# Performance work log

Hardware: AMD Instinct MI355X
Metric: run time of the kernel (lower is better)

## Reference

```python
import jax, jax.numpy as jnp
import numpy as np

D_MODEL = 1024
N_HEAD = 16
DK = D_MODEL // N_HEAD
D_FF = 2048
EPS = 1e-6
NEG = -1e10


def layer_norm(x, gamma, beta):
    # torch .std() is unbiased (N-1), and eps is added to std (not var)
    mean = jnp.mean(x, axis=-1, keepdims=True)
    var = jnp.sum((x - mean) ** 2, axis=-1, keepdims=True) / (x.shape[-1] - 1)
    std = jnp.sqrt(var)
    return gamma * (x - mean) / (std + EPS) + beta


def setup_inputs() -> dict:
    key = jax.random.key(0)
    ks = jax.random.split(key, 12)
    s = 0.02
    inp = {
        'x': jax.random.normal(ks[0], (16, 512, D_MODEL), dtype=jnp.float32),
        'x_mask': jax.random.randint(ks[1], (16, 1, 1, 512), 0, 2, dtype=jnp.int32),
        'Wq': jax.random.normal(ks[2], (D_MODEL, D_MODEL), dtype=jnp.float32) * s,
        'bq': jnp.zeros((D_MODEL,), jnp.float32),
        'Wk': jax.random.normal(ks[3], (D_MODEL, D_MODEL), dtype=jnp.float32) * s,
        'bk': jnp.zeros((D_MODEL,), jnp.float32),
        'Wv': jax.random.normal(ks[4], (D_MODEL, D_MODEL), dtype=jnp.float32) * s,
        'bv': jnp.zeros((D_MODEL,), jnp.float32),
        'Wo': jax.random.normal(ks[5], (D_MODEL, D_MODEL), dtype=jnp.float32) * s,
        'bo': jnp.zeros((D_MODEL,), jnp.float32),
        'gamma1': jnp.ones((D_MODEL,), jnp.float32),
        'beta1': jnp.zeros((D_MODEL,), jnp.float32),
        'W1': jax.random.normal(ks[6], (D_MODEL, D_FF), dtype=jnp.float32) * s,
        'b1': jnp.zeros((D_FF,), jnp.float32),
        'W2': jax.random.normal(ks[7], (D_FF, D_MODEL), dtype=jnp.float32) * s,
        'b2': jnp.zeros((D_MODEL,), jnp.float32),
        'gamma2': jnp.ones((D_MODEL,), jnp.float32),
        'beta2': jnp.zeros((D_MODEL,), jnp.float32),
    }
    return inp


def reference(x, x_mask, Wq, bq, Wk, bk, Wv, bv, Wo, bo, gamma1, beta1,
              W1, b1, W2, b2, gamma2, beta2):
    B, S, _ = x.shape
    # QKV projections -> [B, S, H, DK]
    q = (x @ Wq + bq).reshape(B, S, N_HEAD, DK)
    k = (x @ Wk + bk).reshape(B, S, N_HEAD, DK)
    v = (x @ Wv + bv).reshape(B, S, N_HEAD, DK)
    # scores [B, H, Sq, Sk]
    scores = jnp.einsum('bqhd,bkhd->bhqk', q, k) / jnp.sqrt(jnp.float32(DK))
    scores = jnp.where(x_mask == 0, jnp.float32(NEG), scores)
    probs = jax.nn.softmax(scores, axis=-1)
    attn = jnp.einsum('bhqk,bkhd->bqhd', probs, v).reshape(B, S, D_MODEL)
    attn_out = attn @ Wo + bo
    # residual + post-LN 1
    h = layer_norm(attn_out + x, gamma1, beta1)
    # FFN (exact GELU as torch nn.GELU default)
    ffn = jax.nn.gelu(h @ W1 + b1, approximate=False) @ W2 + b2
    out = layer_norm(ffn + h, gamma2, beta2)
    return out
```

## Files before the change

kernel.cpp:

```cpp
#include <hip/hip_runtime.h>
#include <math.h>

#define B_ 16
#define S_ 512
#define DM 1024
#define NH 16
#define DFF 2048

typedef short bf16x8 __attribute__((ext_vector_type(8)));
typedef float f32x4 __attribute__((ext_vector_type(4)));
typedef unsigned short u16;

__device__ __forceinline__ u16 f2bf(float f) {
  unsigned int u = __float_as_uint(f);
  u += 0x7FFF + ((u >> 16) & 1);
  return (u16)(u >> 16);
}

__device__ __forceinline__ unsigned cvtpk_bf16(float lo, float hi) {
  unsigned r;
  asm("v_cvt_pk_bf16_f32 %0, %1, %2" : "=v"(r) : "v"(lo), "v"(hi));
  return r;
}

__device__ __forceinline__ float gelu_exact(float x) {
  return 0.5f * x * (1.0f + erff(x * 0.70710678118654752f));
}

__device__ __forceinline__ void gload_lds16(const void* g, void* l) {
  __builtin_amdgcn_global_load_lds((const __attribute__((address_space(1))) void*)g,
                                   (__attribute__((address_space(3))) void*)l, 16, 0, 0);
}

#define QSCALE 0.18033688011112042f
#define MASKNEG -1.442695e10f


__global__ void cvt_bf16_k(const float* __restrict__ in, u16* __restrict__ out, int n) {
  int i = (blockIdx.x * blockDim.x + threadIdx.x) * 4;
  float4 v = *(const float4*)(in + i);
  uint2 pk;
  pk.x = (unsigned)f2bf(v.x) | ((unsigned)f2bf(v.y) << 16);
  pk.y = (unsigned)f2bf(v.z) | ((unsigned)f2bf(v.w) << 16);
  *(uint2*)(out + i) = pk;
}

__global__ void transpose_bf16(const float* __restrict__ W, u16* __restrict__ Wt, int K, int N) {
  __shared__ float tile[32][33];
  int n0 = blockIdx.x * 32, k0 = blockIdx.y * 32;
  int tx = threadIdx.x, ty = threadIdx.y;
#pragma unroll
  for (int j = 0; j < 32; j += 8)
    tile[ty + j][tx] = W[(size_t)(k0 + ty + j) * N + n0 + tx];
  __syncthreads();
#pragma unroll
  for (int j = 0; j < 32; j += 8)
    Wt[(size_t)(n0 + ty + j) * K + k0 + tx] = f2bf(tile[tx][ty + j]);
}

__global__ void bias_cat(const float* __restrict__ bq, const float* __restrict__ bk,
                         const float* __restrict__ bv, float* __restrict__ o) {
  int i = blockIdx.x * 256 + threadIdx.x;
  o[i] = (i < 1024) ? bq[i] : ((i < 2048) ? bk[i - 1024] : bv[i - 2048]);
}

template <int EPI>
__global__ __launch_bounds__(256, 2)
void gemm_mfma(const u16* __restrict__ A, const u16* __restrict__ Bt,
               const float* __restrict__ bias, void* __restrict__ Cout,
               u16* __restrict__ vT, int M, int N, int K) {
  __shared__ __align__(16) char lds[73728];
  const int tid = threadIdx.x;
  const int w = tid >> 6, lane = tid & 63;
  const int wm = w >> 1, wn = w & 1;

  const int gx = gridDim.x;
  const int nwg = gx * gridDim.y;
  const int lin = blockIdx.y * gx + blockIdx.x;
  const int wg = (lin & 7) * (nwg >> 3) + (lin >> 3);
  const int bm = wg / gx, bn = wg % gx;

  const int NT = K >> 5;

  const int srow = w * 16 + (lane >> 2);
  const int skel = ((lane & 3) ^ (lane >> 4)) * 8;
  const u16* gA = A + (size_t)(bm * 256 + srow) * K + skel;
  const u16* gB = Bt + (size_t)(bn * 128 + srow) * K + skel;
  const size_t rs64 = (size_t)64 * K;
  const int dstb = w * 1024;

  const int lr = lane & 15, kg = lane >> 4;
  const int kslot = (kg ^ ((lr >> 2) & 3)) << 4;
  const int fAoff = (wm * 128 + lr) * 64 + kslot;
  const int fBoff = 16384 + (wn * 64 + lr) * 64 + kslot;

  f32x4 acc[8][4];
#pragma unroll
  for (int i = 0; i < 8; ++i)
#pragma unroll
    for (int j = 0; j < 4; ++j) acc[i][j] = (f32x4){0.f, 0.f, 0.f, 0.f};

#define STAGE_A(t_, sl_)                                         \
  do {                                                           \
    const u16* g_ = gA + (size_t)(t_) * 32;                      \
    char* d_ = lds + (sl_) * 24576 + dstb;                       \
    gload_lds16(g_, d_);                                         \
    gload_lds16(g_ + rs64, d_ + 4096);                           \
    gload_lds16(g_ + 2 * rs64, d_ + 8192);                       \
    gload_lds16(g_ + 3 * rs64, d_ + 12288);                      \
  } while (0)
#define STAGE_B(t_, sl_)                                         \
  do {                                                           \
    const u16* g_ = gB + (size_t)(t_) * 32;                      \
    char* d_ = lds + (sl_) * 24576 + 16384 + dstb;               \
    gload_lds16(g_, d_);                                         \
    gload_lds16(g_ + rs64, d_ + 4096);                           \
  } while (0)

  STAGE_A(0, 0);
  STAGE_B(0, 0);
  STAGE_A(1, 1);
  STAGE_B(1, 1);
  asm volatile("s_waitcnt vmcnt(6)" ::: "memory");
  __builtin_amdgcn_s_barrier();
  __builtin_amdgcn_sched_barrier(0);

  int cs = 0, ss = 2;
  for (int t = 0; t < NT; ++t) {
    const int st = (t + 2 < NT) ? (t + 2) : (NT - 1);
    const char* fA = lds + cs * 24576 + fAoff;
    const char* fB = lds + cs * 24576 + fBoff;
    bf16x8 av[4], bv[4];
#pragma unroll
    for (int mi = 0; mi < 4; ++mi) av[mi] = *(const bf16x8*)(fA + mi * 1024);
#pragma unroll
    for (int ni = 0; ni < 4; ++ni) bv[ni] = *(const bf16x8*)(fB + ni * 1024);
    STAGE_A(st, ss);
    __builtin_amdgcn_s_setprio(1);
#pragma unroll
    for (int mi = 0; mi < 4; ++mi)
#pragma unroll
      for (int ni = 0; ni < 4; ++ni)
        acc[mi][ni] = __builtin_amdgcn_mfma_f32_16x16x32_bf16(av[mi], bv[ni], acc[mi][ni], 0, 0, 0);
    __builtin_amdgcn_s_setprio(0);
    bf16x8 av2[4];
#pragma unroll
    for (int mi = 0; mi < 4; ++mi) av2[mi] = *(const bf16x8*)(fA + 4096 + mi * 1024);
    STAGE_B(st, ss);
    __builtin_amdgcn_s_setprio(1);
#pragma unroll
    for (int mi = 0; mi < 4; ++mi)
#pragma unroll
      for (int ni = 0; ni < 4; ++ni)
        acc[4 + mi][ni] = __builtin_amdgcn_mfma_f32_16x16x32_bf16(av2[mi], bv[ni], acc[4 + mi][ni], 0, 0, 0);
    __builtin_amdgcn_s_setprio(0);
    asm volatile("s_waitcnt vmcnt(6) lgkmcnt(0)" ::: "memory");
    __builtin_amdgcn_s_barrier();
    __builtin_amdgcn_sched_barrier(0);
    cs = (cs == 2) ? 0 : cs + 1;
    ss = (ss == 2) ? 0 : ss + 1;
  }
#undef STAGE_A
#undef STAGE_B

  const int crow0 = bm * 256 + wm * 128;
  const int ccol0 = bn * 128 + wn * 64;
#pragma unroll
  for (int mi = 0; mi < 8; ++mi) {
#pragma unroll
    for (int ni = 0; ni < 4; ++ni) {
      const int col = ccol0 + ni * 16 + lr;
      const float bv = bias[col];
      const int rowb = crow0 + mi * 16 + (lane >> 4) * 4;
      float v[4];
#pragma unroll
      for (int r = 0; r < 4; ++r) v[r] = acc[mi][ni][r] + bv;
      if (EPI == 1) {
#pragma unroll
        for (int r = 0; r < 4; ++r)
          ((u16*)Cout)[(size_t)(rowb + r) * N + col] = f2bf(gelu_exact(v[r]));
      } else if (EPI == 2) {
#pragma unroll
        for (int r = 0; r < 4; ++r)
          ((float*)Cout)[(size_t)(rowb + r) * N + col] = v[r];
      } else {
        if (col < 2048) {
          const float sc = (col < 1024) ? QSCALE : 1.0f;
#pragma unroll
          for (int r = 0; r < 4; ++r)
            ((u16*)Cout)[(size_t)(rowb + r) * 2048 + col] = f2bf(v[r] * sc);
        } else {
          const int b = rowb >> 9, s = rowb & 511;
          const int hd = col - 2048;
          ushort4 pk;
          pk.x = f2bf(v[0]); pk.y = f2bf(v[1]); pk.z = f2bf(v[2]); pk.w = f2bf(v[3]);
          *(ushort4*)(vT + ((size_t)(b * NH + (hd >> 6)) * 64 + (hd & 63)) * S_ + s) = pk;
        }
      }
    }
  }
}

__global__ __launch_bounds__(256, 3)
void attn_kernel(const u16* __restrict__ qk,
                 const u16* __restrict__ vT,
                 const int* __restrict__ mask,
                 u16* __restrict__ out) {
  __shared__ __align__(16) u16 Qs[32 * 72];
  __shared__ __align__(16) u16 Pl[32 * 520];
  __shared__ __align__(16) float Mlf[512];
  __shared__ __align__(16) float Rsum[32][4];

  const int tid = threadIdx.x;
  const int w = tid >> 6, lane = tid & 63;
  const int bid = blockIdx.x;
  const int widx = (bid & 7) * 512 + (bid >> 3);
  const int qt = widx & 15, h = (widx >> 4) & 15, b = widx >> 8;
  const int q0 = qt * 32;
  const int arow = lane & 15, kg = lane >> 4;

  {
    int r = tid >> 3, slot = tid & 7;
    bf16x8 v = *(const bf16x8*)(qk + (size_t)(b * S_ + q0 + r) * 2048 + h * 64 + slot * 8);
    *(bf16x8*)((char*)Qs + r * 144 + slot * 16) = v;
  }
  Mlf[tid] = (mask[b * S_ + tid] == 0) ? MASKNEG : 0.f;
  Mlf[tid + 256] = (mask[b * S_ + tid + 256] == 0) ? MASKNEG : 0.f;
  __syncthreads();

  bf16x8 qf[2][2];
#pragma unroll
  for (int mi = 0; mi < 2; ++mi)
#pragma unroll
    for (int kk = 0; kk < 2; ++kk)
      qf[mi][kk] = *(const bf16x8*)((char*)Qs + (mi * 16 + arow) * 144 + kk * 64 + kg * 16);

  f32x4 s0[8], s1[8];
  const u16* kbase = qk + (size_t)(b * S_) * 2048 + 1024 + h * 64 + kg * 8;
#pragma unroll
  for (int half = 0; half < 2; ++half) {
    bf16x8 kvl[4][2];
#pragma unroll
    for (int j = 0; j < 4; ++j) {
      const int colg = w * 128 + (half * 4 + j) * 16 + arow;
      const u16* kr = kbase + (size_t)colg * 2048;
      kvl[j][0] = *(const bf16x8*)(kr);
      kvl[j][1] = *(const bf16x8*)(kr + 32);
    }
#pragma unroll
    for (int j = 0; j < 4; ++j) {
      const int ni = half * 4 + j;
      f32x4 a0 = {0.f, 0.f, 0.f, 0.f}, a1 = {0.f, 0.f, 0.f, 0.f};
      a0 = __builtin_amdgcn_mfma_f32_16x16x32_bf16(kvl[j][0], qf[0][0], a0, 0, 0, 0);
      a0 = __builtin_amdgcn_mfma_f32_16x16x32_bf16(kvl[j][1], qf[0][1], a0, 0, 0, 0);
      a1 = __builtin_amdgcn_mfma_f32_16x16x32_bf16(kvl[j][0], qf[1][0], a1, 0, 0, 0);
      a1 = __builtin_amdgcn_mfma_f32_16x16x32_bf16(kvl[j][1], qf[1][1], a1, 0, 0, 0);
      const f32x4 mb = *(const f32x4*)&Mlf[w * 128 + ni * 16 + kg * 4];
      s0[ni] = a0 + mb;
      s1[ni] = a1 + mb;
    }
  }

  const u16* vb = vT + ((size_t)(b * NH + h) * 64 + w * 16 + arow) * S_ + kg * 8;
  bf16x8 vv[8];
#pragma unroll
  for (int i = 0; i < 8; ++i) vv[i] = *(const bf16x8*)(vb + i * 32);

  f32x4 ac0 = {0.f, 0.f, 0.f, 0.f}, ac1 = ac0;
#pragma unroll
  for (int ni = 0; ni < 8; ++ni) {
#pragma unroll
    for (int r = 0; r < 4; ++r) {
      s0[ni][r] = __builtin_amdgcn_exp2f(s0[ni][r]);
      s1[ni][r] = __builtin_amdgcn_exp2f(s1[ni][r]);
    }
    ac0 += s0[ni];
    ac1 += s1[ni];
  }
  float t0 = ac0[0] + ac0[1] + ac0[2] + ac0[3];
  float t1 = ac1[0] + ac1[1] + ac1[2] + ac1[3];
  t0 += __shfl_xor(t0, 16);
  t0 += __shfl_xor(t0, 32);
  t1 += __shfl_xor(t1, 16);
  t1 += __shfl_xor(t1, 32);
  if (kg == 0) {
    Rsum[arow][w] = t0;
    Rsum[16 + arow][w] = t1;
  }

  {
    const int kq = w * 128 + kg * 4;
    char* const p0 = (char*)Pl + (arow * 520 + kq) * 2;
    char* const p1 = (char*)Pl + ((16 + arow) * 520 + kq) * 2;
#pragma unroll
    for (int ni = 0; ni < 8; ++ni) {
      uint2 pk;
      pk.x = cvtpk_bf16(s0[ni][0], s0[ni][1]);
      pk.y = cvtpk_bf16(s0[ni][2], s0[ni][3]);
      *(uint2*)(p0 + ni * 32) = pk;
      pk.x = cvtpk_bf16(s1[ni][0], s1[ni][1]);
      pk.y = cvtpk_bf16(s1[ni][2], s1[ni][3]);
      *(uint2*)(p1 + ni * 32) = pk;
    }
  }
  __syncthreads();

  {
    f32x4 oa[2];
    oa[0] = (f32x4){0.f, 0.f, 0.f, 0.f};
    oa[1] = (f32x4){0.f, 0.f, 0.f, 0.f};
#pragma unroll
    for (int t16 = 0; t16 < 16; ++t16) {
      const int sk0 = t16 * 32;
      bf16x8 bfr = (t16 < 8) ? vv[t16] : *(const bf16x8*)(vb + t16 * 32);
#pragma unroll
      for (int mi = 0; mi < 2; ++mi) {
        bf16x8 pa = *(const bf16x8*)(Pl + (mi * 16 + arow) * 520 + sk0 + kg * 8);
        oa[mi] = __builtin_amdgcn_mfma_f32_16x16x32_bf16(pa, bfr, oa[mi], 0, 0, 0);
      }
    }
#pragma unroll
    for (int mi = 0; mi < 2; ++mi)
#pragma unroll
      for (int r = 0; r < 4; ++r) {
        const int rloc = mi * 16 + kg * 4 + r;
        f32x4 sv = *(const f32x4*)&Rsum[rloc][0];
        const float inv = 1.0f / (sv[0] + sv[1] + sv[2] + sv[3]);
        const int qrow = q0 + rloc;
        out[(size_t)(b * S_ + qrow) * DM + h * 64 + w * 16 + arow] = f2bf(oa[mi][r] * inv);
      }
  }
}

__global__ __launch_bounds__(256)
void ln_kernel(const float* __restrict__ a, const float* __restrict__ res,
               const float* __restrict__ gamma, const float* __restrict__ beta,
               float* __restrict__ out, u16* __restrict__ outb) {
  const int row = blockIdx.x, tid = threadIdx.x;
  const int w = tid >> 6, lane = tid & 63;
  const size_t base = (size_t)row * DM + tid * 4;
  float4 va = *(const float4*)(a + base);
  float4 vr = *(const float4*)(res + base);
  float v0 = va.x + vr.x, v1 = va.y + vr.y, v2 = va.z + vr.z, v3 = va.w + vr.w;
  float s = v0 + v1 + v2 + v3;
  float ss = v0 * v0 + v1 * v1 + v2 * v2 + v3 * v3;
#pragma unroll
  for (int off = 32; off >= 1; off >>= 1) {
    s += __shfl_down(s, off);
    ss += __shfl_down(ss, off);
  }
  __shared__ float ps[4], pss[4], mb[2];
  if (lane == 0) { ps[w] = s; pss[w] = ss; }
  __syncthreads();
  if (tid == 0) {
    float S = ps[0] + ps[1] + ps[2] + ps[3];
    float SS = pss[0] + pss[1] + pss[2] + pss[3];
    float mean = S * (1.0f / DM);
    float var = (SS - (float)DM * mean * mean) * (1.0f / (DM - 1));
    var = fmaxf(var, 0.f);
    mb[0] = mean;
    mb[1] = 1.0f / (sqrtf(var) + 1e-6f);
  }
  __syncthreads();
  const float mean = mb[0], rinv = mb[1];
  const int c = tid * 4;
  float y0 = gamma[c] * (v0 - mean) * rinv + beta[c];
  float y1 = gamma[c + 1] * (v1 - mean) * rinv + beta[c + 1];
  float y2 = gamma[c + 2] * (v2 - mean) * rinv + beta[c + 2];
  float y3 = gamma[c + 3] * (v3 - mean) * rinv + beta[c + 3];
  float4 o = {y0, y1, y2, y3};
  *(float4*)(out + base) = o;
  if (outb) {
    uint2 pk;
    pk.x = (unsigned)f2bf(y0) | ((unsigned)f2bf(y1) << 16);
    pk.y = (unsigned)f2bf(y2) | ((unsigned)f2bf(y3) << 16);
    *(uint2*)(outb + base) = pk;
  }
}


extern "C" void kernel_launch(void* const* d_in, const int* in_sizes, int n_in,
                              void* d_out, int out_size, void* d_ws, size_t ws_size,
                              hipStream_t stream) {
  const float* x = (const float*)d_in[0];
  const int* xm = (const int*)d_in[1];
  const float* Wq = (const float*)d_in[2];
  const float* bq = (const float*)d_in[3];
  const float* Wk = (const float*)d_in[4];
  const float* bk = (const float*)d_in[5];
  const float* Wv = (const float*)d_in[6];
  const float* bv = (const float*)d_in[7];
  const float* Wo = (const float*)d_in[8];
  const float* bo = (const float*)d_in[9];
  const float* g1 = (const float*)d_in[10];
  const float* be1 = (const float*)d_in[11];
  const float* W1 = (const float*)d_in[12];
  const float* b1 = (const float*)d_in[13];
  const float* W2 = (const float*)d_in[14];
  const float* b2 = (const float*)d_in[15];
  const float* g2 = (const float*)d_in[16];
  const float* be2 = (const float*)d_in[17];

  char* ws = (char*)d_ws;
  u16* xb = (u16*)(ws);
  u16* wqkvt = (u16*)(ws + 16777216);
  u16* wot = (u16*)(ws + 23068672);
  u16* w1t = (u16*)(ws + 25165824);
  u16* w2t = (u16*)(ws + 29360128);
  float* bqkv = (float*)(ws + 33554432);
  u16* qkb = (u16*)(ws + 33566720);
  u16* vtb = (u16*)(ws + 67121152);
  u16* attnb = (u16*)(ws + 83898368);
  float* f32a = (float*)(ws + 100675584);
  float* hbuf = (float*)(ws + 134230016);
  u16* hb = xb;

  cvt_bf16_k<<<dim3(8192), dim3(256), 0, stream>>>(x, xb, 8388608);
  transpose_bf16<<<dim3(32, 32), dim3(32, 8), 0, stream>>>(Wq, wqkvt, 1024, 1024);
  transpose_bf16<<<dim3(32, 32), dim3(32, 8), 0, stream>>>(Wk, wqkvt + 1024 * 1024, 1024, 1024);
  transpose_bf16<<<dim3(32, 32), dim3(32, 8), 0, stream>>>(Wv, wqkvt + 2 * 1024 * 1024, 1024, 1024);
  transpose_bf16<<<dim3(32, 32), dim3(32, 8), 0, stream>>>(Wo, wot, 1024, 1024);
  transpose_bf16<<<dim3(64, 32), dim3(32, 8), 0, stream>>>(W1, w1t, 1024, 2048);
  transpose_bf16<<<dim3(32, 64), dim3(32, 8), 0, stream>>>(W2, w2t, 2048, 1024);
  bias_cat<<<dim3(12), dim3(256), 0, stream>>>(bq, bk, bv, bqkv);

  gemm_mfma<3><<<dim3(24, 32), dim3(256), 0, stream>>>(xb, wqkvt, bqkv, (void*)qkb, vtb, 8192, 3072, 1024);
  attn_kernel<<<dim3(4096), dim3(256), 0, stream>>>(qkb, vtb, xm, attnb);
  gemm_mfma<2><<<dim3(8, 32), dim3(256), 0, stream>>>(attnb, wot, bo, (void*)f32a, (u16*)nullptr, 8192, 1024, 1024);
  ln_kernel<<<dim3(8192), dim3(256), 0, stream>>>(f32a, x, g1, be1, hbuf, hb);
  gemm_mfma<1><<<dim3(16, 32), dim3(256), 0, stream>>>(hb, w1t, b1, (void*)qkb, (u16*)nullptr, 8192, 2048, 1024);
  gemm_mfma<2><<<dim3(8, 32), dim3(256), 0, stream>>>(qkb, w2t, b2, (void*)f32a, (u16*)nullptr, 8192, 1024, 2048);
  ln_kernel<<<dim3(8192), dim3(256), 0, stream>>>(f32a, hbuf, g2, be2, (float*)d_out, (u16*)nullptr);
}
```

Measured before the change: 316.5 us.

## Store GEMM outputs and LN residual in bf16, hoist V loads in attention

The Wo and W2 GEMMs now write bf16 instead of fp32 intermediates. The layer-norm kernel is templated to read bf16 inputs and to write only the outputs it needs. The second layer norm takes its residual from the bf16 copy of h instead of a separate fp32 h buffer, which removes the fp32 hbuf write and read. In the attention kernel, the V fragment loads move before the first barrier so they overlap the QK work. The cost is lower precision in the pre-LN sums and in the residual.

```diff
diff --git a/kernel.cpp b/kernel.cpp
--- a/kernel.cpp
+++ b/kernel.cpp
@@ -15,6 +15,10 @@
   unsigned int u = __float_as_uint(f);
   u += 0x7FFF + ((u >> 16) & 1);
   return (u16)(u >> 16);
+}
+
+__device__ __forceinline__ float bf2f(u16 u) {
+  return __uint_as_float(((unsigned)u) << 16);
 }
 
 __device__ __forceinline__ unsigned cvtpk_bf16(float lo, float hi) {
@@ -183,6 +187,10 @@
 #pragma unroll
         for (int r = 0; r < 4; ++r)
           ((float*)Cout)[(size_t)(rowb + r) * N + col] = v[r];
+      } else if (EPI == 4) {
+#pragma unroll
+        for (int r = 0; r < 4; ++r)
+          ((u16*)Cout)[(size_t)(rowb + r) * N + col] = f2bf(v[r]);
       } else {
         if (col < 2048) {
           const float sc = (col < 1024) ? QSCALE : 1.0f;
@@ -226,6 +234,12 @@
   }
   Mlf[tid] = (mask[b * S_ + tid] == 0) ? MASKNEG : 0.f;
   Mlf[tid + 256] = (mask[b * S_ + tid + 256] == 0) ? MASKNEG : 0.f;
+
+  const u16* vb = vT + ((size_t)(b * NH + h) * 64 + w * 16 + arow) * S_ + kg * 8;
+  bf16x8 vv[8];
+#pragma unroll
+  for (int i = 0; i < 8; ++i) vv[i] = *(const bf16x8*)(vb + i * 32);
+
   __syncthreads();
 
   bf16x8 qf[2][2];
@@ -261,11 +275,6 @@
     }
   }
 
-  const u16* vb = vT + ((size_t)(b * NH + h) * 64 + w * 16 + arow) * S_ + kg * 8;
-  bf16x8 vv[8];
-#pragma unroll
-  for (int i = 0; i < 8; ++i) vv[i] = *(const bf16x8*)(vb + i * 32);
-
   f32x4 ac0 = {0.f, 0.f, 0.f, 0.f}, ac1 = ac0;
 #pragma unroll
   for (int ni = 0; ni < 8; ++ni) {
@@ -332,16 +341,33 @@
   }
 }
 
+template <int AB, int RB, int WF, int WB>
 __global__ __launch_bounds__(256)
-void ln_kernel(const float* __restrict__ a, const float* __restrict__ res,
+void ln_kernel(const void* __restrict__ a, const void* __restrict__ res,
                const float* __restrict__ gamma, const float* __restrict__ beta,
-               float* __restrict__ out, u16* __restrict__ outb) {
+               float* __restrict__ outf, u16* __restrict__ outb) {
   const int row = blockIdx.x, tid = threadIdx.x;
   const int w = tid >> 6, lane = tid & 63;
   const size_t base = (size_t)row * DM + tid * 4;
-  float4 va = *(const float4*)(a + base);
-  float4 vr = *(const float4*)(res + base);
-  float v0 = va.x + vr.x, v1 = va.y + vr.y, v2 = va.z + vr.z, v3 = va.w + vr.w;
+  float v0, v1, v2, v3;
+  {
+    float a0, a1, a2, a3, r0, r1, r2, r3;
+    if (AB) {
+      ushort4 u = *(const ushort4*)((const u16*)a + base);
+      a0 = bf2f(u.x); a1 = bf2f(u.y); a2 = bf2f(u.z); a3 = bf2f(u.w);
+    } else {
+      float4 u = *(const float4*)((const float*)a + base);
+      a0 = u.x; a1 = u.y; a2 = u.z; a3 = u.w;
+    }
+    if (RB) {
+      ushort4 u = *(const ushort4*)((const u16*)res + base);
+      r0 = bf2f(u.x); r1 = bf2f(u.y); r2 = bf2f(u.z); r3 = bf2f(u.w);
+    } else {
+      float4 u = *(const float4*)((const float*)res + base);
+      r0 = u.x; r1 = u.y; r2 = u.z; r3 = u.w;
+    }
+    v0 = a0 + r0; v1 = a1 + r1; v2 = a2 + r2; v3 = a3 + r3;
+  }
   float s = v0 + v1 + v2 + v3;
   float ss = v0 * v0 + v1 * v1 + v2 * v2 + v3 * v3;
 #pragma unroll
@@ -368,9 +394,11 @@
   float y1 = gamma[c + 1] * (v1 - mean) * rinv + beta[c + 1];
   float y2 = gamma[c + 2] * (v2 - mean) * rinv + beta[c + 2];
   float y3 = gamma[c + 3] * (v3 - mean) * rinv + beta[c + 3];
-  float4 o = {y0, y1, y2, y3};
-  *(float4*)(out + base) = o;
-  if (outb) {
+  if (WF) {
+    float4 o = {y0, y1, y2, y3};
+    *(float4*)(outf + base) = o;
+  }
+  if (WB) {
     uint2 pk;
     pk.x = (unsigned)f2bf(y0) | ((unsigned)f2bf(y1) << 16);
     pk.y = (unsigned)f2bf(y2) | ((unsigned)f2bf(y3) << 16);
@@ -411,8 +439,8 @@
   u16* qkb = (u16*)(ws + 33566720);
   u16* vtb = (u16*)(ws + 67121152);
   u16* attnb = (u16*)(ws + 83898368);
-  float* f32a = (float*)(ws + 100675584);
-  float* hbuf = (float*)(ws + 134230016);
+  u16* attnpb = (u16*)(ws + 100675584);
+  u16* f2b = (u16*)(ws + 117452800);
   u16* hb = xb;
 
   cvt_bf16_k<<<dim3(8192), dim3(256), 0, stream>>>(x, xb, 8388608);
@@ -426,9 +454,9 @@
 
   gemm_mfma<3><<<dim3(24, 32), dim3(256), 0, stream>>>(xb, wqkvt, bqkv, (void*)qkb, vtb, 8192, 3072, 1024);
   attn_kernel<<<dim3(4096), dim3(256), 0, stream>>>(qkb, vtb, xm, attnb);
-  gemm_mfma<2><<<dim3(8, 32), dim3(256), 0, stream>>>(attnb, wot, bo, (void*)f32a, (u16*)nullptr, 8192, 1024, 1024);
-  ln_kernel<<<dim3(8192), dim3(256), 0, stream>>>(f32a, x, g1, be1, hbuf, hb);
+  gemm_mfma<4><<<dim3(8, 32), dim3(256), 0, stream>>>(attnb, wot, bo, (void*)attnpb, (u16*)nullptr, 8192, 1024, 1024);
+  ln_kernel<1, 0, 0, 1><<<dim3(8192), dim3(256), 0, stream>>>(attnpb, x, g1, be1, (float*)nullptr, hb);
   gemm_mfma<1><<<dim3(16, 32), dim3(256), 0, stream>>>(hb, w1t, b1, (void*)qkb, (u16*)nullptr, 8192, 2048, 1024);
-  gemm_mfma<2><<<dim3(8, 32), dim3(256), 0, stream>>>(qkb, w2t, b2, (void*)f32a, (u16*)nullptr, 8192, 1024, 2048);
-  ln_kernel<<<dim3(8192), dim3(256), 0, stream>>>(f32a, hbuf, g2, be2, (float*)d_out, (u16*)nullptr);
-}
+  gemm_mfma<4><<<dim3(8, 32), dim3(256), 0, stream>>>(qkb, w2t, b2, (void*)f2b, (u16*)nullptr, 8192, 1024, 2048);
+  ln_kernel<1, 1, 1, 0><<<dim3(8192), dim3(256), 0, stream>>>(f2b, hb, g2, be2, (float*)d_out, (u16*)nullptr);
+}
```

Result: faster. 305.9 us (-3.3%).
